# Performance work log

Hardware: AMD Instinct MI355X
Metric: run time of the kernel (lower is better)

## Reference

```python
import jax, jax.numpy as jnp
import numpy as np

N = 100000      # nodes
E = 800000      # edges (before self loops)
D_IN = 128
D_H = 128
HEADS = 8
HD = D_H // HEADS   # per-head dim for hidden layers
D_OUT = 64
SLOPE = 0.2         # PyG GATConv default negative_slope
EPS_BN = 1e-5
EPS_LN = 1e-5


def setup_inputs() -> dict:
    key = jax.random.key(0)
    ks = jax.random.split(key, 20)
    def p(k, shape, scale=0.1):
        return jax.random.normal(k, shape, dtype=jnp.float32) * scale
    inp = {
        "x": jax.random.normal(ks[0], (N, D_IN), dtype=jnp.float32),
        "edge_index": jax.random.randint(ks[1], (2, E), 0, N, dtype=jnp.int32),
        # GATConv 0: 128 -> 8 heads x 16, concat -> 128
        "W0": p(ks[2], (D_IN, D_H)), "as0": p(ks[3], (HEADS, HD)), "ad0": p(ks[4], (HEADS, HD)),
        "b0": jnp.zeros((D_H,), jnp.float32),
        "g0": jnp.ones((D_H,), jnp.float32), "bt0": jnp.zeros((D_H,), jnp.float32),
        # GATConv 1: 128 -> 8 heads x 16, concat -> 128
        "W1": p(ks[5], (D_H, D_H)), "as1": p(ks[6], (HEADS, HD)), "ad1": p(ks[7], (HEADS, HD)),
        "b1": jnp.zeros((D_H,), jnp.float32),
        "g1": jnp.ones((D_H,), jnp.float32), "bt1": jnp.zeros((D_H,), jnp.float32),
        # GATConv 2 (final): 128 -> 1 head x 64, no concat
        "W2": p(ks[8], (D_H, D_OUT)), "as2": p(ks[9], (1, D_OUT)), "ad2": p(ks[10], (1, D_OUT)),
        "b2": jnp.zeros((D_OUT,), jnp.float32),
        # output LayerNorm
        "ln_g": jnp.ones((D_OUT,), jnp.float32), "ln_b": jnp.zeros((D_OUT,), jnp.float32),
    }
    return inp


def gat_conv(x, src, dst, W, a_s, a_d, heads):
    """PyG-style GATConv (eval mode, self loops already in src/dst).
    Returns [N, heads, head_dim]."""
    n = x.shape[0]
    h = (x @ W).reshape(n, heads, -1)              # [N, H, D]
    al_s = jnp.sum(h * a_s, axis=-1)               # [N, H]
    al_d = jnp.sum(h * a_d, axis=-1)               # [N, H]
    e = jax.nn.leaky_relu(al_s[src] + al_d[dst], SLOPE)  # [Etot, H]
    # softmax over incoming edges of each destination node
    m = jax.ops.segment_max(e, dst, num_segments=n)
    e = jnp.exp(e - m[dst])
    s = jax.ops.segment_sum(e, dst, num_segments=n)
    alpha = e / (s[dst] + 1e-16)                   # [Etot, H]
    msg = h[src] * alpha[:, :, None]               # [Etot, H, D]
    return jax.ops.segment_sum(msg, dst, num_segments=n)


def batch_norm(x, g, b):
    mu = jnp.mean(x, axis=0)
    var = jnp.var(x, axis=0)
    return (x - mu) * jax.lax.rsqrt(var + EPS_BN) * g + b


def reference(x, edge_index, W0, as0, ad0, b0, g0, bt0,
              W1, as1, ad1, b1, g1, bt1,
              W2, as2, ad2, b2, ln_g, ln_b):
    n = x.shape[0]
    loops = jnp.arange(n, dtype=edge_index.dtype)
    src = jnp.concatenate([edge_index[0], loops])
    dst = jnp.concatenate([edge_index[1], loops])

    # layer 0
    out = gat_conv(x, src, dst, W0, as0, ad0, HEADS).reshape(n, D_H) + b0
    out = jax.nn.relu(batch_norm(out, g0, bt0))
    x = out + x                                    # residual (128 == 128)

    # layer 1
    out = gat_conv(x, src, dst, W1, as1, ad1, HEADS).reshape(n, D_H) + b1
    out = jax.nn.relu(batch_norm(out, g1, bt1))
    x = out + x

    # final layer: 1 head, concat=False
    out = gat_conv(x, src, dst, W2, as2, ad2, 1).reshape(n, D_OUT) + b2

    # output LayerNorm
    mu = jnp.mean(out, axis=-1, keepdims=True)
    var = jnp.var(out, axis=-1, keepdims=True)
    return (out - mu) * jax.lax.rsqrt(var + EPS_LN) * ln_g + ln_b
```

## Files before the change

### kernel.cpp

```cpp
#include <hip/hip_runtime.h>
#include <hip/hip_bf16.h>

#define LRELU(e) ((e) > 0.f ? (e) : 0.2f * (e))

typedef __attribute__((ext_vector_type(8))) short bf16x8;
typedef __attribute__((ext_vector_type(4))) float floatx4;

__device__ inline short f2bf(float f) {
    union { float f; unsigned u; } v; v.f = f;
    unsigned r = v.u + 0x7fffu + ((v.u >> 16) & 1u);
    return (short)(r >> 16);
}
__device__ inline float bflo(int p) {
    union { unsigned u; float f; } v; v.u = (unsigned)p << 16; return v.f;
}
__device__ inline float bfhi(int p) {
    union { unsigned u; float f; } v; v.u = (unsigned)p & 0xffff0000u; return v.f;
}
__device__ inline float bf2f(unsigned short s) {
    union { unsigned u; float f; } v; v.u = (unsigned)s << 16; return v.f;
}


__global__ void k_count_wprep(const int* __restrict__ dstE, int E, int N,
                              int* __restrict__ deg,
                              const float* __restrict__ W0, const float* __restrict__ W1,
                              const float* __restrict__ W2,
                              const float* __restrict__ as0, const float* __restrict__ ad0,
                              const float* __restrict__ as1, const float* __restrict__ ad1,
                              const float* __restrict__ as2, const float* __restrict__ ad2,
                              short* __restrict__ Wt0, short* __restrict__ Wt1,
                              short* __restrict__ Wt2) {
    int i = blockIdx.x * blockDim.x + threadIdx.x;
    if (i < E) atomicAdd(&deg[dstE[i]], 1);
    else if (i < E + N) atomicAdd(&deg[i - E], 1);

    if (i < 128 * 128) {
        int n = i >> 7, k = i & 127;
        Wt0[n * 128 + k] = f2bf(W0[k * 128 + n]);
        Wt1[n * 128 + k] = f2bf(W1[k * 128 + n]);
    } else if (i < 128 * 128 + 64 * 128) {
        int j = i - 128 * 128;
        int n = j >> 7, k = j & 127;
        Wt2[n * 128 + k] = f2bf(W2[k * 64 + n]);
    } else if (i < 128 * 128 + 64 * 128 + 128 * 8) {
        int j = i - (128 * 128 + 64 * 128);
        int k = j >> 3, h = j & 7;
        float s0 = 0.f, d0 = 0.f, s1 = 0.f, d1 = 0.f;
        #pragma unroll
        for (int d = 0; d < 16; d++) {
            float w0 = W0[k * 128 + h * 16 + d];
            float w1 = W1[k * 128 + h * 16 + d];
            s0 += w0 * as0[h * 16 + d];
            d0 += w0 * ad0[h * 16 + d];
            s1 += w1 * as1[h * 16 + d];
            d1 += w1 * ad1[h * 16 + d];
        }
        Wt0[(128 + h) * 128 + k] = f2bf(s0);
        Wt0[(136 + h) * 128 + k] = f2bf(d0);
        Wt1[(128 + h) * 128 + k] = f2bf(s1);
        Wt1[(136 + h) * 128 + k] = f2bf(d1);
    } else if (i < 128 * 128 + 64 * 128 + 128 * 8 + 128) {
        int k = i - (128 * 128 + 64 * 128 + 128 * 8);
        float s = 0.f, d = 0.f;
        #pragma unroll
        for (int dd = 0; dd < 64; dd++) {
            float w = W2[k * 64 + dd];
            s += w * as2[dd];
            d += w * ad2[dd];
        }
        Wt2[64 * 128 + k] = f2bf(s);
        Wt2[65 * 128 + k] = f2bf(d);
        #pragma unroll
        for (int r = 66; r < 80; r++) Wt2[r * 128 + k] = 0;
    }
}

constexpr int SC = 2048;

__global__ __launch_bounds__(256) void k_scan1(const int* __restrict__ deg, int N,
                                               int* __restrict__ partial) {
    int base = blockIdx.x * SC;
    int t = threadIdx.x;
    int s = 0;
    #pragma unroll
    for (int p = 0; p < SC / 256; p++) {
        int i = base + t + p * 256;
        if (i < N) s += deg[i];
    }
    #pragma unroll
    for (int off = 32; off; off >>= 1) s += __shfl_xor(s, off, 64);
    __shared__ int ws[4];
    int lane = t & 63, wid = t >> 6;
    if (lane == 0) ws[wid] = s;
    __syncthreads();
    if (t == 0) partial[blockIdx.x] = ws[0] + ws[1] + ws[2] + ws[3];
}

__global__ __launch_bounds__(256) void k_scan2(int* __restrict__ partial, int nb) {
    int t = threadIdx.x;
    int v = (t < nb) ? partial[t] : 0;
    int lane = t & 63, wid = t >> 6;
    int x = v;
    #pragma unroll
    for (int off = 1; off < 64; off <<= 1) {
        int y = __shfl_up(x, off, 64);
        if (lane >= off) x += y;
    }
    __shared__ int wsum[4];
    if (lane == 63) wsum[wid] = x;
    __syncthreads();
    int add = 0;
    for (int i = 0; i < wid; i++) add += wsum[i];
    if (t < nb) partial[t] = x + add - v;
}


__global__ __launch_bounds__(256) void k_scan3(const int* __restrict__ deg, int N, int Etot,
                                               const int* __restrict__ partial,
                                               int* __restrict__ rowptr,
                                               int* __restrict__ bcursor) {
    int base = blockIdx.x * SC;
    int t = threadIdx.x;
    int i0 = base + t * 8;
    int v[8];
    int s = 0;
    #pragma unroll
    for (int p = 0; p < 8; p++) {
        int i = i0 + p;
        v[p] = (i < N) ? deg[i] : 0;
        s += v[p];
    }
    int lane = t & 63, wid = t >> 6;
    int x = s;
    #pragma unroll
    for (int off = 1; off < 64; off <<= 1) {
        int y = __shfl_up(x, off, 64);
        if (lane >= off) x += y;
    }
    __shared__ int wsum[4];
    if (lane == 63) wsum[wid] = x;
    __syncthreads();
    int add = 0;
    for (int i = 0; i < wid; i++) add += wsum[i];
    int excl = x - s + add + partial[blockIdx.x];
    #pragma unroll
    for (int p = 0; p < 8; p++) {
        int i = i0 + p;
        if (i < N) {
            rowptr[i] = excl;
            if ((i & 127) == 0) bcursor[i >> 7] = excl - i;
        }
        excl += v[p];
    }
    if (blockIdx.x == 0 && t == 0) rowptr[N] = Etot;
}


constexpr int EPT = 16;

__global__ __launch_bounds__(256) void k_bin(const int* __restrict__ srcE,
                                             const int* __restrict__ dstE, int E, int nb,
                                             int* __restrict__ bcursor,
                                             int2* __restrict__ ebin) {
    __shared__ int cnt[1024];
    __shared__ int base[1024];
    for (int b = threadIdx.x; b < nb; b += 256) cnt[b] = 0;
    __syncthreads();
    int i0 = blockIdx.x * (256 * EPT) + threadIdx.x;
    int rb[EPT];
    #pragma unroll
    for (int k = 0; k < EPT; k++) {
        int i = i0 + k * 256;
        if (i < E) {
            int b = dstE[i] >> 7;
            rb[k] = (atomicAdd(&cnt[b], 1) << 10) | b;
        } else {
            rb[k] = -1;
        }
    }
    __syncthreads();
    for (int b = threadIdx.x; b < nb; b += 256) {
        int c = cnt[b];
        base[b] = c ? atomicAdd(&bcursor[b], c) : 0;
    }
    __syncthreads();
    #pragma unroll
    for (int k = 0; k < EPT; k++) {
        int i = i0 + k * 256;
        if (i < E) {
            int v = rb[k];
            int b = v & 1023;
            int r = v >> 10;
            ebin[base[b] + r] = make_int2(srcE[i], dstE[i]);
        }
    }
}


__global__ __launch_bounds__(256) void k_cfill(const int* __restrict__ rowptr,
                                               const int2* __restrict__ ebin,
                                               int* __restrict__ col, int N) {
    int n0 = blockIdx.x << 7;
    int nn = N - n0; if (nn > 128) nn = 128;
    __shared__ int cur[128];
    __shared__ int eb[2];
    int t = threadIdx.x;
    if (t <= nn) {
        int rp = rowptr[n0 + t];
        if (t < nn) {
            col[rp] = n0 + t;
            cur[t] = rp + 1;
        }
        if (t == 0) eb[0] = rp - n0;
        if (t == nn) eb[1] = rp - (n0 + nn);
    }
    __syncthreads();
    int ebase = eb[0];
    int ecnt = eb[1] - ebase;
    for (int i = t; i < ecnt; i += 256) {
        int2 e = ebin[ebase + i];
        int p = atomicAdd(&cur[e.y - n0], 1);
        col[p] = e.x;
    }
}


template <int DOUT, bool HASBN, bool RESBF16, bool WRITEX>
__global__ __launch_bounds__(256) void k_gemm(const void* __restrict__ Xv,
                                              const short* __restrict__ Wt,
                                              short* __restrict__ Hout,
                                              const float2* __restrict__ ss,
                                              const void* __restrict__ Xresv,
                                              short* __restrict__ Xout,
                                              float* __restrict__ als,
                                              float* __restrict__ ald, int Nrows) {
    constexpr int KP = 136;
    constexpr int CT = DOUT / 16;
    constexpr int CTT = CT + 1;
    __shared__ __align__(16) short Xs[128 * KP];
    __shared__ __align__(16) short Ws[(DOUT + 16) * KP];

    const int tid = threadIdx.x;
    const int row0 = blockIdx.x * 128;

    {
        int c4 = tid & 31;
        int r0 = tid >> 5;
        float2 ssv[4];
        if (HASBN) {
            #pragma unroll
            for (int j = 0; j < 4; j++) ssv[j] = ss[c4 * 4 + j];
        }
        #pragma unroll
        for (int p = 0; p < 16; p++) {
            int r = r0 + p * 8;
            int grow = row0 + r;
            float vp[4] = {0.f, 0.f, 0.f, 0.f};
            if (grow < Nrows) {
                if (HASBN) {
                    short4 xb = *(const short4*)&((const short*)Xv)[(size_t)grow * 128 + c4 * 4];
                    vp[0] = bf2f((unsigned short)xb.x);
                    vp[1] = bf2f((unsigned short)xb.y);
                    vp[2] = bf2f((unsigned short)xb.z);
                    vp[3] = bf2f((unsigned short)xb.w);
                    float xr[4];
                    if (RESBF16) {
                        short4 rb = *(const short4*)&((const short*)Xresv)[(size_t)grow * 128 + c4 * 4];
                        xr[0] = bf2f((unsigned short)rb.x);
                        xr[1] = bf2f((unsigned short)rb.y);
                        xr[2] = bf2f((unsigned short)rb.z);
                        xr[3] = bf2f((unsigned short)rb.w);
                    } else {
                        float4 rf = *(const float4*)&((const float*)Xresv)[(size_t)grow * 128 + c4 * 4];
                        xr[0] = rf.x; xr[1] = rf.y; xr[2] = rf.z; xr[3] = rf.w;
                    }
                    #pragma unroll
                    for (int j = 0; j < 4; j++)
                        vp[j] = fmaxf(vp[j] * ssv[j].x + ssv[j].y, 0.f) + xr[j];
                } else {
                    float4 v = *(const float4*)&((const float*)Xv)[(size_t)grow * 128 + c4 * 4];
                    vp[0] = v.x; vp[1] = v.y; vp[2] = v.z; vp[3] = v.w;
                }
            }
            short4 b;
            b.x = f2bf(vp[0]); b.y = f2bf(vp[1]); b.z = f2bf(vp[2]); b.w = f2bf(vp[3]);
            if (WRITEX && grow < Nrows)
                *(short4*)&Xout[(size_t)grow * 128 + c4 * 4] = b;
            *(short4*)&Xs[r * KP + c4 * 4] = b;
        }
    }
    {
        constexpr int UNITS = (DOUT + 16) * 16;
        #pragma unroll
        for (int p = 0; p < UNITS / 256; p++) {
            int u = tid + p * 256;
            int n = u >> 4;
            int kc = (u & 15) * 8;
            bf16x8 v = *(const bf16x8*)&Wt[n * 128 + kc];
            *(bf16x8*)&Ws[n * KP + kc] = v;
        }
    }
    __syncthreads();

    const int lane = tid & 63;
    const int wv = tid >> 6;
    const int m0 = wv * 32;
    const int ln = lane & 15;
    const int quad = lane >> 4;

    floatx4 acc[2][CTT];
    #pragma unroll
    for (int mt = 0; mt < 2; mt++)
        #pragma unroll
        for (int ct = 0; ct < CTT; ct++) acc[mt][ct] = (floatx4){0.f, 0.f, 0.f, 0.f};

    #pragma unroll
    for (int ks = 0; ks < 4; ks++) {
        int ko = ks * 32 + quad * 8;
        bf16x8 a0 = *(const bf16x8*)&Xs[(m0 + ln) * KP + ko];
        bf16x8 a1 = *(const bf16x8*)&Xs[(m0 + 16 + ln) * KP + ko];
        #pragma unroll
        for (int ct = 0; ct < CTT; ct++) {
            bf16x8 b = *(const bf16x8*)&Ws[(ct * 16 + ln) * KP + ko];
            acc[0][ct] = __builtin_amdgcn_mfma_f32_16x16x32_bf16(a0, b, acc[0][ct], 0, 0, 0);
            acc[1][ct] = __builtin_amdgcn_mfma_f32_16x16x32_bf16(a1, b, acc[1][ct], 0, 0, 0);
        }
    }

    #pragma unroll
    for (int mt = 0; mt < 2; mt++) {
        #pragma unroll
        for (int r = 0; r < 4; r++) {
            int grow = row0 + m0 + mt * 16 + quad * 4 + r;
            if (grow < Nrows) {
                #pragma unroll
                for (int ct = 0; ct < CT; ct++)
                    Hout[(size_t)grow * DOUT + ct * 16 + ln] = f2bf(acc[mt][ct][r]);
                float aug = acc[mt][CT][r];
                if (DOUT == 128) {
                    if (ln < 8) als[grow * 8 + ln] = aug;
                    else        ald[grow * 8 + (ln - 8)] = aug;
                } else {
                    if (ln == 0) als[grow] = aug;
                    else if (ln == 1) ald[grow] = aug;
                }
            }
        }
    }
}


__global__ __launch_bounds__(256) void k_agg(const int* __restrict__ rowptr,
                                             const int* __restrict__ col,
                                             const short* __restrict__ Hb,
                                             const float* __restrict__ als,
                                             const float* __restrict__ ald,
                                             const float* __restrict__ bias,
                                             short* __restrict__ out,
                                             float* __restrict__ part, int N) {
    __shared__ float red[8][128];
    const int wv = threadIdx.x >> 6;
    const int lane = threadIdx.x & 63;
    const int g = lane >> 5;
    const int f = lane & 31;
    const int h = f >> 2;
    const int node = blockIdx.x * 8 + wv * 2 + g;
    const int2* H2 = (const int2*)Hb;

    int j = 0, deg = 0;
    float aldv = 0.f;
    if (node < N) {
        j = rowptr[node];
        deg = rowptr[node + 1] - j;
        aldv = ald[node * 8 + h];
    }
    float s = 0.f, a0 = 0.f, a1 = 0.f, a2 = 0.f, a3 = 0.f;

    int done = 0;
    while (__any(done < deg)) {
        int take = deg - done;
        if (take > 32) take = 32;
        int li = (f < take) ? f : (take - 1);
        if (li < 0) li = 0;
        int cbuf = col[j + done + li];
        for (int k = 0; __any(k < take); k += 4) {
            int c0 = __shfl(cbuf, k, 32);
            int c1 = __shfl(cbuf, k + 1, 32);
            int c2 = __shfl(cbuf, k + 2, 32);
            int c3 = __shfl(cbuf, k + 3, 32);
            float aw0 = als[c0 * 8 + h];
            float aw1 = als[c1 * 8 + h];
            float aw2 = als[c2 * 8 + h];
            float aw3 = als[c3 * 8 + h];
            int2 p0 = H2[(c0 << 5) + f];
            int2 p1 = H2[(c1 << 5) + f];
            int2 p2 = H2[(c2 << 5) + f];
            int2 p3 = H2[(c3 << 5) + f];
            float e0 = aw0 + aldv; e0 = LRELU(e0);
            float e1 = aw1 + aldv; e1 = LRELU(e1);
            float e2 = aw2 + aldv; e2 = LRELU(e2);
            float e3 = aw3 + aldv; e3 = LRELU(e3);
            float w0 = (k     < take) ? __expf(e0) : 0.f;
            float w1 = (k + 1 < take) ? __expf(e1) : 0.f;
            float w2 = (k + 2 < take) ? __expf(e2) : 0.f;
            float w3 = (k + 3 < take) ? __expf(e3) : 0.f;
            s += w0;
            a0 += w0 * bflo(p0.x); a1 += w0 * bfhi(p0.x);
            a2 += w0 * bflo(p0.y); a3 += w0 * bfhi(p0.y);
            s += w1;
            a0 += w1 * bflo(p1.x); a1 += w1 * bfhi(p1.x);
            a2 += w1 * bflo(p1.y); a3 += w1 * bfhi(p1.y);
            s += w2;
            a0 += w2 * bflo(p2.x); a1 += w2 * bfhi(p2.x);
            a2 += w2 * bflo(p2.y); a3 += w2 * bfhi(p2.y);
            s += w3;
            a0 += w3 * bflo(p3.x); a1 += w3 * bfhi(p3.x);
            a2 += w3 * bflo(p3.y); a3 += w3 * bfhi(p3.y);
        }
        done += take;
    }

    float o0 = 0.f, o1 = 0.f, o2 = 0.f, o3 = 0.f;
    if (node < N) {
        float4 bv = ((const float4*)bias)[f];
        float inv = 1.f / (s + 1e-16f);
        o0 = a0 * inv + bv.x;
        o1 = a1 * inv + bv.y;
        o2 = a2 * inv + bv.z;
        o3 = a3 * inv + bv.w;
        int2 pk;
        pk.x = (int)((unsigned short)f2bf(o0) | ((unsigned)(unsigned short)f2bf(o1) << 16));
        pk.y = (int)((unsigned short)f2bf(o2) | ((unsigned)(unsigned short)f2bf(o3) << 16));
        ((int2*)out)[(size_t)node * 32 + f] = pk;
    }
    const int rrow = wv * 2 + g;
    red[rrow][4 * f + 0] = o0;
    red[rrow][4 * f + 1] = o1;
    red[rrow][4 * f + 2] = o2;
    red[rrow][4 * f + 3] = o3;
    __syncthreads();
    if (threadIdx.x < 128) {
        int c = threadIdx.x;
        float s2 = 0.f, q = 0.f;
        #pragma unroll
        for (int r = 0; r < 8; r++) {
            float v = red[r][c];
            s2 += v;
            q += v * v;
        }
        float* slot = part + (blockIdx.x & 63) * 256;
        atomicAdd(&slot[c], s2);
        atomicAdd(&slot[128 + c], q);
    }
}


__global__ __launch_bounds__(128) void k_bnreduce(float* __restrict__ part,
                                                  const float* __restrict__ g,
                                                  const float* __restrict__ bt,
                                                  float invN, float2* __restrict__ ss) {
    int c = threadIdx.x;
    float s = 0.f, q = 0.f;
    #pragma unroll
    for (int k = 0; k < 64; k++) {
        s += part[k * 256 + c];
        q += part[k * 256 + 128 + c];
    }
    #pragma unroll
    for (int k = 0; k < 64; k++) {
        part[k * 256 + c] = 0.f;
        part[k * 256 + 128 + c] = 0.f;
    }
    float mu = s * invN;
    float var = q * invN - mu * mu;
    float scale = rsqrtf(var + 1e-5f) * g[c];
    ss[c] = make_float2(scale, bt[c] - mu * scale);
}


__global__ __launch_bounds__(256) void k_agg2ln(const int* __restrict__ rowptr,
                                                const int* __restrict__ col,
                                                const short* __restrict__ Hb2,
                                                const float* __restrict__ als,
                                                const float* __restrict__ ald,
                                                const float* __restrict__ b2,
                                                const float* __restrict__ lng,
                                                const float* __restrict__ lnb,
                                                float* __restrict__ out, int N) {
    const int wv = threadIdx.x >> 6;
    const int lane = threadIdx.x & 63;
    const int g = lane >> 5;
    const int f = lane & 31;
    const int node = blockIdx.x * 8 + wv * 2 + g;
    const int* H1 = (const int*)Hb2;
    const bool vn = node < N;

    int j = 0, deg = 0;
    float aldv = 0.f;
    if (vn) {
        j = rowptr[node];
        deg = rowptr[node + 1] - j;
        aldv = ald[node];
    }
    float s = 0.f, a0 = 0.f, a1 = 0.f;

    int done = 0;
    while (__any(done < deg)) {
        int take = deg - done;
        if (take > 32) take = 32;
        int li = (f < take) ? f : (take - 1);
        if (li < 0) li = 0;
        int cbuf = col[j + done + li];
        for (int k = 0; __any(k < take); k += 4) {
            int c0 = __shfl(cbuf, k, 32);
            int c1 = __shfl(cbuf, k + 1, 32);
            int c2 = __shfl(cbuf, k + 2, 32);
            int c3 = __shfl(cbuf, k + 3, 32);
            float aw0 = als[c0];
            float aw1 = als[c1];
            float aw2 = als[c2];
            float aw3 = als[c3];
            int p0 = H1[(c0 << 5) + f];
            int p1 = H1[(c1 << 5) + f];
            int p2 = H1[(c2 << 5) + f];
            int p3 = H1[(c3 << 5) + f];
            float e0 = aw0 + aldv; e0 = LRELU(e0);
            float e1 = aw1 + aldv; e1 = LRELU(e1);
            float e2 = aw2 + aldv; e2 = LRELU(e2);
            float e3 = aw3 + aldv; e3 = LRELU(e3);
            float w0 = (k     < take) ? __expf(e0) : 0.f;
            float w1 = (k + 1 < take) ? __expf(e1) : 0.f;
            float w2 = (k + 2 < take) ? __expf(e2) : 0.f;
            float w3 = (k + 3 < take) ? __expf(e3) : 0.f;
            s += w0; a0 += w0 * bflo(p0); a1 += w0 * bfhi(p0);
            s += w1; a0 += w1 * bflo(p1); a1 += w1 * bfhi(p1);
            s += w2; a0 += w2 * bflo(p2); a1 += w2 * bfhi(p2);
            s += w3; a0 += w3 * bflo(p3); a1 += w3 * bfhi(p3);
        }
        done += take;
    }

    if (!vn) return;
    float inv = 1.f / (s + 1e-16f);
    float2 bv = ((const float2*)b2)[f];
    float v0 = a0 * inv + bv.x;
    float v1 = a1 * inv + bv.y;
    float su = v0 + v1, sq = v0 * v0 + v1 * v1;
    #pragma unroll
    for (int off = 1; off < 32; off <<= 1) {
        su += __shfl_xor(su, off, 64);
        sq += __shfl_xor(sq, off, 64);
    }
    float mu = su * (1.f / 64.f);
    float var = sq * (1.f / 64.f) - mu * mu;
    float r = rsqrtf(var + 1e-5f);
    float2 lg = ((const float2*)lng)[f];
    float2 lb = ((const float2*)lnb)[f];
    float2 ov;
    ov.x = (v0 - mu) * r * lg.x + lb.x;
    ov.y = (v1 - mu) * r * lg.y + lb.y;
    ((float2*)out)[(size_t)node * 32 + f] = ov;
}


extern "C" void kernel_launch(void* const* d_in, const int* in_sizes, int n_in,
                              void* d_out, int out_size, void* d_ws, size_t ws_size,
                              hipStream_t stream) {
    const float* x   = (const float*)d_in[0];
    const int*   ei  = (const int*)d_in[1];
    const float* W0  = (const float*)d_in[2];
    const float* as0 = (const float*)d_in[3];
    const float* ad0 = (const float*)d_in[4];
    const float* b0  = (const float*)d_in[5];
    const float* g0  = (const float*)d_in[6];
    const float* bt0 = (const float*)d_in[7];
    const float* W1  = (const float*)d_in[8];
    const float* as1 = (const float*)d_in[9];
    const float* ad1 = (const float*)d_in[10];
    const float* b1  = (const float*)d_in[11];
    const float* g1  = (const float*)d_in[12];
    const float* bt1 = (const float*)d_in[13];
    const float* W2  = (const float*)d_in[14];
    const float* as2 = (const float*)d_in[15];
    const float* ad2 = (const float*)d_in[16];
    const float* b2  = (const float*)d_in[17];
    const float* lng = (const float*)d_in[18];
    const float* lnb = (const float*)d_in[19];

    const int N = in_sizes[0] / 128;
    const int E = in_sizes[1] / 2;
    const int Etot = E + N;
    const int nb = (N + 127) >> 7;

    char* p = (char*)d_ws;
    auto carve = [&](size_t bytes) {
        void* q = (void*)p;
        p += (bytes + 255) & ~(size_t)255;
        return q;
    };
    short* Hb     = (short*)carve((size_t)N * 128 * 2);
    short* aggb   = (short*)carve((size_t)N * 128 * 2);
    short* x1b    = (short*)carve((size_t)N * 128 * 2);
    float* als    = (float*)carve((size_t)N * 8 * 4);
    float* ald    = (float*)carve((size_t)N * 8 * 4);
    int*   rowptr = (int*)carve((size_t)(N + 1) * 4);
    const size_t degpad = ((size_t)N * 4 + 255) & ~(size_t)255;
    int*   deg    = (int*)carve(degpad);
    float* part   = (float*)carve(64 * 256 * 4);
    int*   col    = (int*)carve((size_t)Etot * 4);
    int2*  ebin   = (int2*)carve((size_t)E * 8);
    int*   bcursor= (int*)carve(1024 * 4);
    float2* ss    = (float2*)carve(128 * 8);
    short* Wt0    = (short*)carve(144 * 128 * 2);
    short* Wt1    = (short*)carve(144 * 128 * 2);
    short* Wt2    = (short*)carve(80 * 128 * 2);
    int*   partial= (int*)carve(256 * 4);

    const float invN = 1.f / (float)N;
    const int eb = (E + N + 255) / 256;
    const int nsb = (N + SC - 1) / SC;

    hipMemsetAsync(deg, 0, degpad + 64 * 256 * 4, stream);
    k_count_wprep<<<eb, 256, 0, stream>>>(ei + E, E, N, deg, W0, W1, W2,
                                          as0, ad0, as1, ad1, as2, ad2, Wt0, Wt1, Wt2);
    k_scan1<<<nsb, 256, 0, stream>>>(deg, N, partial);
    k_scan2<<<1, 256, 0, stream>>>(partial, nsb);
    k_scan3<<<nsb, 256, 0, stream>>>(deg, N, Etot, partial, rowptr, bcursor);
    const int bb = (E + 256 * EPT - 1) / (256 * EPT);
    k_bin<<<bb, 256, 0, stream>>>(ei, ei + E, E, nb, bcursor, ebin);
    k_cfill<<<nb, 256, 0, stream>>>(rowptr, ebin, col, N);

    const int gb = (N + 127) / 128;
    const int ab = (N + 7) / 8;

    k_gemm<128, false, false, false><<<gb, 256, 0, stream>>>(x, Wt0, Hb, nullptr, nullptr,
                                                             nullptr, als, ald, N);
    k_agg<<<ab, 256, 0, stream>>>(rowptr, col, Hb, als, ald, b0, aggb, part, N);
    k_bnreduce<<<1, 128, 0, stream>>>(part, g0, bt0, invN, ss);

    k_gemm<128, true, false, true><<<gb, 256, 0, stream>>>(aggb, Wt1, Hb, ss, x, x1b,
                                                           als, ald, N);
    k_agg<<<ab, 256, 0, stream>>>(rowptr, col, Hb, als, ald, b1, aggb, part, N);
    k_bnreduce<<<1, 128, 0, stream>>>(part, g1, bt1, invN, ss);

    k_gemm<64, true, true, false><<<gb, 256, 0, stream>>>(aggb, Wt2, Hb, ss, x1b, nullptr,
                                                          als, ald, N);
    k_agg2ln<<<ab, 256, 0, stream>>>(rowptr, col, Hb, als, ald, b2, lng, lnb,
                                     (float*)d_out, N);
}
```

Baseline: 401.9 us.

## Build CSR from per-bucket counts instead of per-node degree atomics and scans

Replaces the global per-node degree atomic count and three-stage scan with a shared-memory bucket count (128 nodes per bucket), a single-block scan over buckets, and a per-bucket local scan inside the column-fill kernel that also writes rowptr. Weight preparation is split into its own small kernel. This removes 900K global atomics and two scan kernels, at the cost of an extra pass over the destination array and a second pass over binned edges in the fill kernel.

```diff
diff --git a/kernel.cpp b/kernel.cpp
--- a/kernel.cpp
+++ b/kernel.cpp
@@ -22,19 +22,19 @@
 }
 
 
-__global__ void k_count_wprep(const int* __restrict__ dstE, int E, int N,
-                              int* __restrict__ deg,
-                              const float* __restrict__ W0, const float* __restrict__ W1,
-                              const float* __restrict__ W2,
-                              const float* __restrict__ as0, const float* __restrict__ ad0,
-                              const float* __restrict__ as1, const float* __restrict__ ad1,
-                              const float* __restrict__ as2, const float* __restrict__ ad2,
-                              short* __restrict__ Wt0, short* __restrict__ Wt1,
-                              short* __restrict__ Wt2) {
+__global__ __launch_bounds__(256) void k_wprep(const float* __restrict__ W0,
+                                               const float* __restrict__ W1,
+                                               const float* __restrict__ W2,
+                                               const float* __restrict__ as0,
+                                               const float* __restrict__ ad0,
+                                               const float* __restrict__ as1,
+                                               const float* __restrict__ ad1,
+                                               const float* __restrict__ as2,
+                                               const float* __restrict__ ad2,
+                                               short* __restrict__ Wt0,
+                                               short* __restrict__ Wt1,
+                                               short* __restrict__ Wt2) {
     int i = blockIdx.x * blockDim.x + threadIdx.x;
-    if (i < E) atomicAdd(&deg[dstE[i]], 1);
-    else if (i < E + N) atomicAdd(&deg[i - E], 1);
-
     if (i < 128 * 128) {
         int n = i >> 7, k = i & 127;
         Wt0[n * 128 + k] = f2bf(W0[k * 128 + n]);
@@ -76,88 +76,64 @@
     }
 }
 
-constexpr int SC = 2048;
-
-__global__ __launch_bounds__(256) void k_scan1(const int* __restrict__ deg, int N,
-                                               int* __restrict__ partial) {
-    int base = blockIdx.x * SC;
+
+constexpr int EPT = 16;
+
+__global__ __launch_bounds__(256) void k_binc(const int* __restrict__ dstE, int E, int nb,
+                                              int* __restrict__ bucket_cnt) {
+    __shared__ int cnt[1024];
+    for (int b = threadIdx.x; b < nb; b += 256) cnt[b] = 0;
+    __syncthreads();
+    int i0 = blockIdx.x * (256 * EPT) + threadIdx.x;
+    #pragma unroll
+    for (int k = 0; k < EPT; k++) {
+        int i = i0 + k * 256;
+        if (i < E) atomicAdd(&cnt[dstE[i] >> 7], 1);
+    }
+    __syncthreads();
+    for (int b = threadIdx.x; b < nb; b += 256) {
+        int c = cnt[b];
+        if (c) atomicAdd(&bucket_cnt[b], c);
+    }
+}
+
+
+__global__ __launch_bounds__(256) void k_scanb(const int* __restrict__ bucket_cnt, int nb,
+                                               int E, int Etot, int N,
+                                               int* __restrict__ ebase,
+                                               int* __restrict__ bcursor,
+                                               int* __restrict__ rowptr) {
     int t = threadIdx.x;
+    int c[4];
     int s = 0;
     #pragma unroll
-    for (int p = 0; p < SC / 256; p++) {
-        int i = base + t + p * 256;
-        if (i < N) s += deg[i];
-    }
-    #pragma unroll
-    for (int off = 32; off; off >>= 1) s += __shfl_xor(s, off, 64);
-    __shared__ int ws[4];
+    for (int i = 0; i < 4; i++) {
+        int b = t * 4 + i;
+        c[i] = (b < nb) ? bucket_cnt[b] : 0;
+        s += c[i];
+    }
     int lane = t & 63, wid = t >> 6;
-    if (lane == 0) ws[wid] = s;
-    __syncthreads();
-    if (t == 0) partial[blockIdx.x] = ws[0] + ws[1] + ws[2] + ws[3];
-}
-
-__global__ __launch_bounds__(256) void k_scan2(int* __restrict__ partial, int nb) {
-    int t = threadIdx.x;
-    int v = (t < nb) ? partial[t] : 0;
-    int lane = t & 63, wid = t >> 6;
-    int x = v;
+    int x = s;
     #pragma unroll
     for (int off = 1; off < 64; off <<= 1) {
         int y = __shfl_up(x, off, 64);
         if (lane >= off) x += y;
     }
-    __shared__ int wsum[4];
-    if (lane == 63) wsum[wid] = x;
+    __shared__ int ws[4];
+    if (lane == 63) ws[wid] = x;
     __syncthreads();
     int add = 0;
-    for (int i = 0; i < wid; i++) add += wsum[i];
-    if (t < nb) partial[t] = x + add - v;
-}
-
-
-__global__ __launch_bounds__(256) void k_scan3(const int* __restrict__ deg, int N, int Etot,
-                                               const int* __restrict__ partial,
-                                               int* __restrict__ rowptr,
-                                               int* __restrict__ bcursor) {
-    int base = blockIdx.x * SC;
-    int t = threadIdx.x;
-    int i0 = base + t * 8;
-    int v[8];
-    int s = 0;
-    #pragma unroll
-    for (int p = 0; p < 8; p++) {
-        int i = i0 + p;
-        v[p] = (i < N) ? deg[i] : 0;
-        s += v[p];
-    }
-    int lane = t & 63, wid = t >> 6;
-    int x = s;
-    #pragma unroll
-    for (int off = 1; off < 64; off <<= 1) {
-        int y = __shfl_up(x, off, 64);
-        if (lane >= off) x += y;
-    }
-    __shared__ int wsum[4];
-    if (lane == 63) wsum[wid] = x;
-    __syncthreads();
-    int add = 0;
-    for (int i = 0; i < wid; i++) add += wsum[i];
-    int excl = x - s + add + partial[blockIdx.x];
-    #pragma unroll
-    for (int p = 0; p < 8; p++) {
-        int i = i0 + p;
-        if (i < N) {
-            rowptr[i] = excl;
-            if ((i & 127) == 0) bcursor[i >> 7] = excl - i;
-        }
-        excl += v[p];
-    }
-    if (blockIdx.x == 0 && t == 0) rowptr[N] = Etot;
-}
-
-
-constexpr int EPT = 16;
+    for (int i = 0; i < wid; i++) add += ws[i];
+    int excl = x - s + add;
+    #pragma unroll
+    for (int i = 0; i < 4; i++) {
+        int b = t * 4 + i;
+        if (b < nb) { ebase[b] = excl; bcursor[b] = excl; }
+        excl += c[i];
+    }
+    if (t == 0) { ebase[nb] = E; rowptr[N] = Etot; }
+}
+
 
 __global__ __launch_bounds__(256) void k_bin(const int* __restrict__ srcE,
                                              const int* __restrict__ dstE, int E, int nb,
@@ -198,29 +174,45 @@
 }
 
 
-__global__ __launch_bounds__(256) void k_cfill(const int* __restrict__ rowptr,
-                                               const int2* __restrict__ ebin,
-                                               int* __restrict__ col, int N) {
-    int n0 = blockIdx.x << 7;
+__global__ __launch_bounds__(256) void k_cfill2(const int* __restrict__ ebase,
+                                                const int2* __restrict__ ebin,
+                                                int* __restrict__ rowptr,
+                                                int* __restrict__ col, int N) {
+    const int b = blockIdx.x;
+    const int n0 = b << 7;
     int nn = N - n0; if (nn > 128) nn = 128;
-    __shared__ int cur[128];
-    __shared__ int eb[2];
-    int t = threadIdx.x;
-    if (t <= nn) {
-        int rp = rowptr[n0 + t];
-        if (t < nn) {
-            col[rp] = n0 + t;
-            cur[t] = rp + 1;
-        }
-        if (t == 0) eb[0] = rp - n0;
-        if (t == nn) eb[1] = rp - (n0 + nn);
-    }
-    __syncthreads();
-    int ebase = eb[0];
-    int ecnt = eb[1] - ebase;
-    for (int i = t; i < ecnt; i += 256) {
-        int2 e = ebin[ebase + i];
-        int p = atomicAdd(&cur[e.y - n0], 1);
+    __shared__ int cnt[128];
+    __shared__ int wtot[2];
+    const int t = threadIdx.x;
+    if (t < 128) cnt[t] = 0;
+    __syncthreads();
+    const int e0 = ebase[b];
+    const int e1 = ebase[b + 1];
+    for (int i = e0 + t; i < e1; i += 256) {
+        atomicAdd(&cnt[ebin[i].y & 127], 1);
+    }
+    __syncthreads();
+    int v = (t < 128) ? cnt[t] : 0;
+    int lane = t & 63;
+    int x = v;
+    #pragma unroll
+    for (int off = 1; off < 64; off <<= 1) {
+        int y = __shfl_up(x, off, 64);
+        if (lane >= off) x += y;
+    }
+    if (t < 128 && lane == 63) wtot[t >> 6] = x;
+    __syncthreads();
+    int excl = x - v + ((t >= 64 && t < 128) ? wtot[0] : 0);
+    if (t < nn) {
+        int rp = e0 + n0 + t + excl;
+        rowptr[n0 + t] = rp;
+        col[rp] = n0 + t;
+        cnt[t] = rp + 1;
+    }
+    __syncthreads();
+    for (int i = e0 + t; i < e1; i += 256) {
+        int2 e = ebin[i];
+        int p = atomicAdd(&cnt[e.y & 127], 1);
         col[p] = e.x;
     }
 }
@@ -605,31 +597,28 @@
     float* als    = (float*)carve((size_t)N * 8 * 4);
     float* ald    = (float*)carve((size_t)N * 8 * 4);
     int*   rowptr = (int*)carve((size_t)(N + 1) * 4);
-    const size_t degpad = ((size_t)N * 4 + 255) & ~(size_t)255;
-    int*   deg    = (int*)carve(degpad);
+    int*   bucket_cnt = (int*)carve(1024 * 4);
     float* part   = (float*)carve(64 * 256 * 4);
     int*   col    = (int*)carve((size_t)Etot * 4);
     int2*  ebin   = (int2*)carve((size_t)E * 8);
+    int*   ebase  = (int*)carve(1028 * 4);
     int*   bcursor= (int*)carve(1024 * 4);
     float2* ss    = (float2*)carve(128 * 8);
     short* Wt0    = (short*)carve(144 * 128 * 2);
     short* Wt1    = (short*)carve(144 * 128 * 2);
     short* Wt2    = (short*)carve(80 * 128 * 2);
-    int*   partial= (int*)carve(256 * 4);
 
     const float invN = 1.f / (float)N;
-    const int eb = (E + N + 255) / 256;
-    const int nsb = (N + SC - 1) / SC;
-
-    hipMemsetAsync(deg, 0, degpad + 64 * 256 * 4, stream);
-    k_count_wprep<<<eb, 256, 0, stream>>>(ei + E, E, N, deg, W0, W1, W2,
-                                          as0, ad0, as1, ad1, as2, ad2, Wt0, Wt1, Wt2);
-    k_scan1<<<nsb, 256, 0, stream>>>(deg, N, partial);
-    k_scan2<<<1, 256, 0, stream>>>(partial, nsb);
-    k_scan3<<<nsb, 256, 0, stream>>>(deg, N, Etot, partial, rowptr, bcursor);
     const int bb = (E + 256 * EPT - 1) / (256 * EPT);
+    const int wpb = (128 * 128 + 64 * 128 + 128 * 8 + 128 + 255) / 256;
+
+    hipMemsetAsync(bucket_cnt, 0, 1024 * 4 + 64 * 256 * 4, stream);
+    k_wprep<<<wpb, 256, 0, stream>>>(W0, W1, W2, as0, ad0, as1, ad1, as2, ad2,
+                                     Wt0, Wt1, Wt2);
+    k_binc<<<bb, 256, 0, stream>>>(ei + E, E, nb, bucket_cnt);
+    k_scanb<<<1, 256, 0, stream>>>(bucket_cnt, nb, E, Etot, N, ebase, bcursor, rowptr);
     k_bin<<<bb, 256, 0, stream>>>(ei, ei + E, E, nb, bcursor, ebin);
-    k_cfill<<<nb, 256, 0, stream>>>(rowptr, ebin, col, N);
+    k_cfill2<<<nb, 256, 0, stream>>>(ebase, ebin, rowptr, col, N);
 
     const int gb = (N + 127) / 128;
     const int ab = (N + 7) / 8;
```

New measurement: 374.7 us. 1.07x faster.
